# Performance work log

Hardware: AMD Instinct MI355X
Metric: run time of the kernel (lower is better)

The kernel has to match this reference:

```python
import jax, jax.numpy as jnp
import numpy as np

B, N, D = 16, 4096, 128
M = 2048  # codebook size
EPS = 1e-10


def setup_inputs() -> dict:
    key = jax.random.key(0)
    kx, kw = jax.random.split(key)
    x = jax.random.normal(kx, (B, N, D), dtype=jnp.float32)
    # codebook (nn.Embedding weight, kaiming-uniform init ~ uniform(-bound, bound))
    bound = np.sqrt(6.0 / D)
    weight = jax.random.uniform(kw, (M, D), dtype=jnp.float32, minval=-bound, maxval=bound)
    return {"x": x, "weight": weight}


def reference(x, weight):
    b, n, d = x.shape
    m = weight.shape[0]
    q = x.reshape(b * n, d)                       # (bn, d)
    # squared L2 distances: ||q||^2 + ||k||^2 - 2 q.k  (temperature==0 -> argmax of -dist)
    l2_q = jnp.sum(q * q, axis=1, keepdims=True)  # (bn, 1)
    l2_k = jnp.sum(weight * weight, axis=1)       # (m,)
    sim = q @ weight.T                            # (bn, m)  GEMM
    dist = l2_q + l2_k - 2.0 * sim
    indices = jnp.argmin(dist, axis=1)            # (bn,)
    z = weight[indices]                           # onehot @ k == gather
    quantized = z.reshape(b, n, d)
    # straight-through estimator (training path): q + (z - q).detach()
    quantized_st = x + jax.lax.stop_gradient(quantized - x)
    # commitment loss: mse(quantized.detach(), x)
    loss = jnp.mean((jax.lax.stop_gradient(quantized_st) - x) ** 2)
    # perplexity over codebook usage (h == 1 head)
    counts = jnp.zeros((m,), dtype=x.dtype).at[indices].add(1.0)
    p = counts / (b * n)                          # mean of onehot over (b, n)
    perp = jnp.exp(-jnp.sum(p * jnp.log(p + EPS)))[None]  # shape (1,) == 'h'
    out_indices = indices.reshape(b, 1, n)
    return quantized_st, loss, perp, out_indices
```

## Files before the change

### kernel.cpp

```cpp
#include <hip/hip_runtime.h>
#include <hip/hip_bf16.h>
#include <math.h>

#define D_DIM 128
#define M_CODES 2048
#define BN_TOT 65536
#define OUT_LOSS 8388608
#define OUT_PERP 8388609
#define OUT_IDX 8388610
#define MARGIN 2e-3f

#define QB 64

#define WS_L2K 0
#define WS_PB 8192
#define WS_IDX 1056768
#define WS_PART 1318912
#define WS_CNT 1351680
#define WS_FLAGCNT 1359872
#define WS_FLAGGED 1360896

typedef __bf16 bf16x8 __attribute__((ext_vector_type(8)));
typedef float f32x4 __attribute__((ext_vector_type(4)));

#define GLOAD_LDS16(g, l)                                         \
  __builtin_amdgcn_global_load_lds(                               \
      (const __attribute__((address_space(1))) void*)(g),         \
      (__attribute__((address_space(3))) void*)(l), 16, 0, 0)

#define MFMA16(a, b, c) __builtin_amdgcn_mfma_f32_16x16x32_bf16((a), (b), (c), 0, 0, 0)

__global__ __launch_bounds__(256) void prep_kernel(const float* __restrict__ w,
                                                   float* __restrict__ l2k,
                                                   __bf16* __restrict__ pb,
                                                   int* __restrict__ counts,
                                                   int* __restrict__ flagcnt) {
  int gid = blockIdx.x * 256 + threadIdx.x;

  if (gid < M_CODES) {
    const float4* p = (const float4*)(w + (size_t)gid * D_DIM);
    double s = 0.0;
#pragma unroll
    for (int j = 0; j < 32; ++j) {
      float4 v = p[j];
      s += (double)(v.x * v.x);
      s += (double)(v.y * v.y);
      s += (double)(v.z * v.z);
      s += (double)(v.w * v.w);
    }
    l2k[gid] = (float)s;
    counts[gid] = 0;
    if (gid == 0) *flagcnt = 0;
  }

  int lane = gid & 63;
  int g = gid >> 6;
  int cid = g & 15;
  int p = g >> 4;
  int k2 = cid & 7;
  int ks = k2 >> 1;
  int wc = k2 & 1;
  int code = p * 32 + wc * 16 + (lane & 15);
  int koff = ks * 32 + (lane >> 4) * 8;
  const float* src = w + (size_t)code * D_DIM + koff;
  float4 u = *(const float4*)src;
  float4 v = *(const float4*)(src + 4);
  float f[8] = {u.x, u.y, u.z, u.w, v.x, v.y, v.z, v.w};
  bf16x8 o;
#pragma unroll
  for (int j = 0; j < 8; ++j) {
    __bf16 hh = (__bf16)f[j];
    o[j] = (cid < 8) ? hh : (__bf16)(f[j] - (float)hh);
  }
  *(bf16x8*)(pb + (size_t)g * 512 + lane * 8) = o;
}

__device__ __forceinline__ void merge_bs(float& b, float& s, int& i,
                                         float ob, float os, int oi) {
  if (ob > b) {
    s = fmaxf(b, os);
    b = ob;
    i = oi;
  } else if (ob < b) {
    s = fmaxf(s, ob);
  } else {
    s = b;
    if (oi < i) i = oi;
  }
}

__global__ __launch_bounds__(256, 2) void argmin_mfma(
    const float* __restrict__ x, const __bf16* __restrict__ pb,
    const float* __restrict__ l2k, int* __restrict__ best_idx,
    int* __restrict__ flag_count, int* __restrict__ flagged) {
  __shared__ __align__(16) unsigned char ldsB[2 * 32768];
  __shared__ float redB[4][32];
  __shared__ float redS[4][32];
  __shared__ int redI[4][32];

  const int tid = threadIdx.x;
  const int wv = tid >> 6;
  const int lane = tid & 63;
  const int col = lane & 15;
  const int quad = lane >> 4;
  const int wc = wv & 1;
  const int wq = wv >> 1;
  const int q0 = blockIdx.x * QB;

  bf16x8 ah[2][4], al[2][4];
#pragma unroll
  for (int mt = 0; mt < 2; ++mt) {
#pragma unroll
    for (int ks = 0; ks < 4; ++ks) {
      const float* xr =
          x + (size_t)(q0 + wq * 32 + 16 * mt + col) * D_DIM + 32 * ks + 8 * quad;
      float4 u = *(const float4*)xr;
      float4 v = *(const float4*)(xr + 4);
      float f[8] = {u.x, u.y, u.z, u.w, v.x, v.y, v.z, v.w};
      bf16x8 h, l;
#pragma unroll
      for (int j = 0; j < 8; ++j) {
        __bf16 hh = (__bf16)f[j];
        h[j] = hh;
        l[j] = (__bf16)(f[j] - (float)hh);
      }
      ah[mt][ks] = h;
      al[mt][ks] = l;
    }
  }

  float m1[2][4], m2[2][4];
  int bp[2][4];
#pragma unroll
  for (int mt = 0; mt < 2; ++mt)
#pragma unroll
    for (int r = 0; r < 4; ++r) {
      m1[mt][r] = -3.4e38f;
      m2[mt][r] = -3.4e38f;
      bp[mt][r] = 0;
    }

  const int ldsw = wc * 1024 + lane * 16;
  const float* l2p = l2k + wc * 16 + col;

  auto stage = [&](int ch, unsigned char* db) {
    const char* s = (const char*)pb + (size_t)ch * 32768 + wv * 8192 + lane * 16;
#pragma unroll
    for (int i = 0; i < 8; ++i) GLOAD_LDS16(s + i * 1024, db + i * 1024);
  };

  stage(0, ldsB + wv * 8192);
  float l2a = l2p[0];
  float l2b = l2p[32];
  __syncthreads();

#pragma unroll 1
  for (int ch = 0; ch < 32; ++ch) {
    const int buf = ch & 1;
    if (ch < 31) stage(ch + 1, ldsB + (buf ^ 1) * 32768 + wv * 8192);
    float l2na = 0.f, l2nb = 0.f;
    if (ch < 31) {
      l2na = l2p[(2 * ch + 2) * 32];
      l2nb = l2p[(2 * ch + 3) * 32];
    }

    const unsigned char* rb = ldsB + buf * 32768 + ldsw;
    float ia = -0.5f * l2a, ib = -0.5f * l2b;
    f32x4 a00 = (f32x4){ia, ia, ia, ia};
    f32x4 a10 = (f32x4){ia, ia, ia, ia};
    f32x4 a01 = (f32x4){ib, ib, ib, ib};
    f32x4 a11 = (f32x4){ib, ib, ib, ib};

    bf16x8 h0 = *(const bf16x8*)(rb);
    bf16x8 l0 = *(const bf16x8*)(rb + 8192);
    bf16x8 h1 = *(const bf16x8*)(rb + 16384);
    bf16x8 l1 = *(const bf16x8*)(rb + 24576);

#define DO_KS(KS, PRE)                                                    \
    {                                                                     \
      bf16x8 nh0, nl0, nh1, nl1;                                          \
      if (PRE) {                                                          \
        nh0 = *(const bf16x8*)(rb + ((KS) + 1) * 2048);                   \
        nl0 = *(const bf16x8*)(rb + 8192 + ((KS) + 1) * 2048);            \
        nh1 = *(const bf16x8*)(rb + 16384 + ((KS) + 1) * 2048);           \
        nl1 = *(const bf16x8*)(rb + 24576 + ((KS) + 1) * 2048);           \
      }                                                                   \
      a00 = MFMA16(al[0][KS], h0, a00);                                   \
      a10 = MFMA16(al[1][KS], h0, a10);                                   \
      a01 = MFMA16(al[0][KS], h1, a01);                                   \
      a11 = MFMA16(al[1][KS], h1, a11);                                   \
      a00 = MFMA16(ah[0][KS], l0, a00);                                   \
      a10 = MFMA16(ah[1][KS], l0, a10);                                   \
      a01 = MFMA16(ah[0][KS], l1, a01);                                   \
      a11 = MFMA16(ah[1][KS], l1, a11);                                   \
      a00 = MFMA16(ah[0][KS], h0, a00);                                   \
      a10 = MFMA16(ah[1][KS], h0, a10);                                   \
      a01 = MFMA16(ah[0][KS], h1, a01);                                   \
      a11 = MFMA16(ah[1][KS], h1, a11);                                   \
      if (PRE) { h0 = nh0; l0 = nl0; h1 = nh1; l1 = nl1; }                \
    }
    DO_KS(0, 1)
    DO_KS(1, 1)
    DO_KS(2, 1)
    DO_KS(3, 0)
#undef DO_KS

#pragma unroll
    for (int mt = 0; mt < 2; ++mt) {
#pragma unroll
      for (int r = 0; r < 4; ++r) {
        float dd = (mt == 0) ? a00[r] : a10[r];
        bool gt = dd > m1[mt][r];
        m2[mt][r] = fmaxf(m2[mt][r], fminf(m1[mt][r], dd));
        bp[mt][r] = gt ? (ch * 2 + 0) : bp[mt][r];
        m1[mt][r] = fmaxf(m1[mt][r], dd);
      }
    }
#pragma unroll
    for (int mt = 0; mt < 2; ++mt) {
#pragma unroll
      for (int r = 0; r < 4; ++r) {
        float dd = (mt == 0) ? a01[r] : a11[r];
        bool gt = dd > m1[mt][r];
        m2[mt][r] = fmaxf(m2[mt][r], fminf(m1[mt][r], dd));
        bp[mt][r] = gt ? (ch * 2 + 1) : bp[mt][r];
        m1[mt][r] = fmaxf(m1[mt][r], dd);
      }
    }

    l2a = l2na;
    l2b = l2nb;
    __syncthreads();
  }

#pragma unroll
  for (int mt = 0; mt < 2; ++mt) {
#pragma unroll
    for (int r = 0; r < 4; ++r) {
      float b = m1[mt][r], s = m2[mt][r];
      int i = bp[mt][r] * 32 + wc * 16 + col;
#pragma unroll
      for (int m = 1; m < 16; m <<= 1) {
        float ob = __shfl_xor(b, m);
        float os = __shfl_xor(s, m);
        int oi = __shfl_xor(i, m);
        merge_bs(b, s, i, ob, os, oi);
      }
      if (col == 0) {
        int qloc = 16 * mt + 4 * quad + r;
        redB[wv][qloc] = b;
        redS[wv][qloc] = s;
        redI[wv][qloc] = i;
      }
    }
  }
  __syncthreads();

  if (tid < QB) {
    int wq2 = tid >> 5;
    int ql = tid & 31;
    float b = -3.4e38f, s = -3.4e38f;
    int i = 0x7fffffff;
    merge_bs(b, s, i, redB[wq2 * 2 + 0][ql], redS[wq2 * 2 + 0][ql], redI[wq2 * 2 + 0][ql]);
    merge_bs(b, s, i, redB[wq2 * 2 + 1][ql], redS[wq2 * 2 + 1][ql], redI[wq2 * 2 + 1][ql]);
    best_idx[q0 + tid] = i;
    if (2.0f * (b - s) < MARGIN) {
      int pos = atomicAdd(flag_count, 1);
      flagged[pos] = q0 + tid;
    }
  }
}

__global__ __launch_bounds__(256) void fixup_kernel(const float* __restrict__ x,
                                                    const float* __restrict__ w,
                                                    const float* __restrict__ l2k32,
                                                    const int* __restrict__ flagged,
                                                    const int* __restrict__ flag_count,
                                                    int* __restrict__ best_idx) {
  __shared__ float qs[D_DIM];
  __shared__ float l2q_sh;
  __shared__ float redD[256];
  __shared__ int redI[256];
  const int tid = threadIdx.x;
  const int n = *flag_count;
  for (int f = blockIdx.x; f < n; f += gridDim.x) {
    __syncthreads();
    int q = flagged[f];
    if (tid < D_DIM) qs[tid] = x[(size_t)q * D_DIM + tid];
    __syncthreads();
    if (tid == 0) {
      double s = 0.0;
      for (int d = 0; d < D_DIM; ++d) {
        float t = qs[d] * qs[d];
        s += (double)t;
      }
      l2q_sh = (float)s;
    }
    __syncthreads();
    const float l2q = l2q_sh;
    float bd = 3.4e38f;
    int bi = 0x7fffffff;
    for (int c = tid; c < M_CODES; c += 256) {
      const float4* wr = (const float4*)(w + (size_t)c * D_DIM);
      double s = 0.0;
#pragma unroll
      for (int j = 0; j < 32; ++j) {
        float4 v = wr[j];
        s = fma((double)qs[j * 4 + 0], (double)v.x, s);
        s = fma((double)qs[j * 4 + 1], (double)v.y, s);
        s = fma((double)qs[j * 4 + 2], (double)v.z, s);
        s = fma((double)qs[j * 4 + 3], (double)v.w, s);
      }
      float simf = (float)s;
      float S = l2q + l2k32[c];
      float T = 2.0f * simf;
      float dist = S - T;
      if (dist < bd) { bd = dist; bi = c; }
    }
    redD[tid] = bd;
    redI[tid] = bi;
    __syncthreads();
    for (int off = 128; off; off >>= 1) {
      if (tid < off) {
        float od = redD[tid + off];
        int oi = redI[tid + off];
        if (od < redD[tid] || (od == redD[tid] && oi < redI[tid])) {
          redD[tid] = od;
          redI[tid] = oi;
        }
      }
      __syncthreads();
    }
    if (tid == 0) best_idx[q] = redI[0];
  }
}

__global__ __launch_bounds__(256) void epilogue_kernel(const float* __restrict__ x,
                                                       const float* __restrict__ w,
                                                       const int* __restrict__ best_idx,
                                                       float* __restrict__ out,
                                                       float* __restrict__ part,
                                                       int* __restrict__ counts) {
  int gid = blockIdx.x * 256 + threadIdx.x;
  int q = gid >> 5;
  int d4 = gid & 31;
  int idx = best_idx[q];
  float4 xv = ((const float4*)x)[gid];
  float4 wv = ((const float4*)w)[(size_t)idx * 32 + d4];
  float4 o;
  float t0 = wv.x - xv.x; o.x = xv.x + t0; float e0 = o.x - xv.x;
  float t1 = wv.y - xv.y; o.y = xv.y + t1; float e1 = o.y - xv.y;
  float t2 = wv.z - xv.z; o.z = xv.z + t2; float e2 = o.z - xv.z;
  float t3 = wv.w - xv.w; o.w = xv.w + t3; float e3 = o.w - xv.w;
  float ls = e0 * e0 + e1 * e1 + e2 * e2 + e3 * e3;
  ((float4*)out)[gid] = o;

  for (int off = 32; off; off >>= 1) ls += __shfl_down(ls, off);
  __shared__ float red[4];
  if ((threadIdx.x & 63) == 0) red[threadIdx.x >> 6] = ls;
  __syncthreads();
  if (threadIdx.x == 0) part[blockIdx.x] = red[0] + red[1] + red[2] + red[3];

  if (d4 == 0) {
    out[OUT_IDX + q] = (float)idx;
    atomicAdd(&counts[idx], 1);
  }
}

__global__ __launch_bounds__(256) void finalize_kernel(const int* __restrict__ counts,
                                                       const float* __restrict__ part,
                                                       float* __restrict__ out) {
  int tid = threadIdx.x;
  float ls = 0.f;
  for (int i = tid; i < 8192; i += 256) ls += part[i];
  float es = 0.f;
  for (int i = tid; i < M_CODES; i += 256) {
    float p = (float)counts[i] * (1.0f / 65536.0f);
    es += p * logf(p + 1e-10f);
  }
  for (int off = 32; off; off >>= 1) {
    ls += __shfl_down(ls, off);
    es += __shfl_down(es, off);
  }
  __shared__ float redl[4], rede[4];
  if ((tid & 63) == 0) {
    redl[tid >> 6] = ls;
    rede[tid >> 6] = es;
  }
  __syncthreads();
  if (tid == 0) {
    out[OUT_LOSS] = (redl[0] + redl[1] + redl[2] + redl[3]) * (1.0f / 8388608.0f);
    out[OUT_PERP] = expf(-(rede[0] + rede[1] + rede[2] + rede[3]));
  }
}

extern "C" void kernel_launch(void* const* d_in, const int* in_sizes, int n_in,
                              void* d_out, int out_size, void* d_ws, size_t ws_size,
                              hipStream_t stream) {
  const float* x = (const float*)d_in[0];
  const float* w = (const float*)d_in[1];
  float* out = (float*)d_out;
  char* ws = (char*)d_ws;
  float* l2k = (float*)(ws + WS_L2K);
  __bf16* pb = (__bf16*)(ws + WS_PB);
  int* bidx = (int*)(ws + WS_IDX);
  float* part = (float*)(ws + WS_PART);
  int* counts = (int*)(ws + WS_CNT);
  int* flagcnt = (int*)(ws + WS_FLAGCNT);
  int* flagged = (int*)(ws + WS_FLAGGED);

  prep_kernel<<<256, 256, 0, stream>>>(w, l2k, pb, counts, flagcnt);
  argmin_mfma<<<BN_TOT / QB, 256, 0, stream>>>(x, pb, l2k, bidx, flagcnt, flagged);
  fixup_kernel<<<256, 256, 0, stream>>>(x, w, l2k, flagged, flagcnt, bidx);
  epilogue_kernel<<<8192, 256, 0, stream>>>(x, w, bidx, out, part, counts);
  finalize_kernel<<<1, 256, 0, stream>>>(counts, part, out);
}
```

Measured before the change: 248.1 us.

## Software-pipeline argmin fold with MFMA and interleave staged loads per k-step

Restructures the main MFMA loop so that the argmin fold of the previous chunk's accumulators runs interleaved with the current chunk's MFMAs, using ping-pong accumulator sets. Global-to-LDS staging of the next chunk is split across the four k-steps with explicit waitcnt, raw s_barrier and sched_barrier plus setprio around MFMA bursts. The codebook norms are pre-scaled by -0.5 into LDS once per block instead of being read from global memory each chunk. It adds more barriers per chunk and higher register pressure from the doubled accumulators.

```diff
diff --git a/kernel.cpp b/kernel.cpp
--- a/kernel.cpp
+++ b/kernel.cpp
@@ -89,11 +89,97 @@
   }
 }
 
+__device__ __forceinline__ void fold4(const f32x4& f, float (&m1r)[4],
+                                      float (&m2r)[4], int (&bpr)[4], int pid) {
+#pragma unroll
+  for (int r = 0; r < 4; ++r) {
+    float dd = f[r];
+    bool gt = dd > m1r[r];
+    m2r[r] = fmaxf(m2r[r], fminf(m1r[r], dd));
+    bpr[r] = gt ? pid : bpr[r];
+    m1r[r] = fmaxf(m1r[r], dd);
+  }
+}
+
+#define MFMA_KS(KS, H0, L0, H1, L1)                                   \
+  A00 = MFMA16(al[0][KS], H0, A00); A10 = MFMA16(al[1][KS], H0, A10); \
+  A01 = MFMA16(al[0][KS], H1, A01); A11 = MFMA16(al[1][KS], H1, A11); \
+  A00 = MFMA16(ah[0][KS], L0, A00); A10 = MFMA16(ah[1][KS], L0, A10); \
+  A01 = MFMA16(ah[0][KS], L1, A01); A11 = MFMA16(ah[1][KS], L1, A11); \
+  A00 = MFMA16(ah[0][KS], H0, A00); A10 = MFMA16(ah[1][KS], H0, A10); \
+  A01 = MFMA16(ah[0][KS], H1, A01); A11 = MFMA16(ah[1][KS], H1, A11);
+
+template <int DOFOLD, int DOSTAGE>
+__device__ __forceinline__ void chunk_body(
+    int CH, int PREV, unsigned char* ldsBp, const char* pbase, int ldsw, int wv,
+    const bf16x8 (&ah)[2][4], const bf16x8 (&al)[2][4],
+    f32x4& A00, f32x4& A10, f32x4& A01, f32x4& A11,
+    const f32x4& F00, const f32x4& F10, const f32x4& F01, const f32x4& F11,
+    float ia, float ib,
+    float (&m1)[2][4], float (&m2)[2][4], int (&bp)[2][4]) {
+  const unsigned char* rb = ldsBp + (CH & 1) * 32768 + ldsw;
+  unsigned char* db = ldsBp + ((CH & 1) ^ 1) * 32768 + wv * 8192;
+  const char* sg = pbase + (size_t)(CH + 1) * 32768;
+
+  if (DOSTAGE) {
+    GLOAD_LDS16(sg, db);
+    GLOAD_LDS16(sg + 1024, db + 1024);
+    asm volatile("s_waitcnt vmcnt(2)" ::: "memory");
+  } else {
+    asm volatile("s_waitcnt vmcnt(0)" ::: "memory");
+  }
+  __builtin_amdgcn_s_barrier();
+  {
+    bf16x8 h0 = *(const bf16x8*)(rb);
+    bf16x8 l0 = *(const bf16x8*)(rb + 8192);
+    bf16x8 h1 = *(const bf16x8*)(rb + 16384);
+    bf16x8 l1 = *(const bf16x8*)(rb + 24576);
+    asm volatile("s_waitcnt lgkmcnt(0)" ::: "memory");
+    __builtin_amdgcn_sched_barrier(0);
+    A00 = (f32x4){ia, ia, ia, ia};
+    A10 = (f32x4){ia, ia, ia, ia};
+    A01 = (f32x4){ib, ib, ib, ib};
+    A11 = (f32x4){ib, ib, ib, ib};
+    __builtin_amdgcn_s_setprio(1);
+    MFMA_KS(0, h0, l0, h1, l1)
+    __builtin_amdgcn_s_setprio(0);
+  }
+  if (DOFOLD) fold4(F00, m1[0], m2[0], bp[0], PREV * 2 + 0);
+  __builtin_amdgcn_s_barrier();
+
+#pragma unroll
+  for (int k = 1; k < 4; ++k) {
+    bf16x8 h0 = *(const bf16x8*)(rb + k * 2048);
+    bf16x8 l0 = *(const bf16x8*)(rb + 8192 + k * 2048);
+    bf16x8 h1 = *(const bf16x8*)(rb + 16384 + k * 2048);
+    bf16x8 l1 = *(const bf16x8*)(rb + 24576 + k * 2048);
+    if (DOSTAGE) {
+      GLOAD_LDS16(sg + (2 * k) * 1024, db + (2 * k) * 1024);
+      GLOAD_LDS16(sg + (2 * k + 1) * 1024, db + (2 * k + 1) * 1024);
+    }
+    __builtin_amdgcn_s_barrier();
+    asm volatile("s_waitcnt lgkmcnt(0)" ::: "memory");
+    __builtin_amdgcn_sched_barrier(0);
+    __builtin_amdgcn_s_setprio(1);
+    if (k == 1) { MFMA_KS(1, h0, l0, h1, l1) }
+    else if (k == 2) { MFMA_KS(2, h0, l0, h1, l1) }
+    else { MFMA_KS(3, h0, l0, h1, l1) }
+    __builtin_amdgcn_s_setprio(0);
+    if (DOFOLD) {
+      if (k == 1) fold4(F10, m1[1], m2[1], bp[1], PREV * 2 + 0);
+      else if (k == 2) fold4(F01, m1[0], m2[0], bp[0], PREV * 2 + 1);
+      else fold4(F11, m1[1], m2[1], bp[1], PREV * 2 + 1);
+    }
+    __builtin_amdgcn_s_barrier();
+  }
+}
+
 __global__ __launch_bounds__(256, 2) void argmin_mfma(
     const float* __restrict__ x, const __bf16* __restrict__ pb,
     const float* __restrict__ l2k, int* __restrict__ best_idx,
     int* __restrict__ flag_count, int* __restrict__ flagged) {
   __shared__ __align__(16) unsigned char ldsB[2 * 32768];
+  __shared__ float l2s[2048];
   __shared__ float redB[4][32];
   __shared__ float redS[4][32];
   __shared__ int redI[4][32];
@@ -129,6 +215,15 @@
     }
   }
 
+  {
+    float4 a = ((const float4*)l2k)[2 * tid];
+    float4 b = ((const float4*)l2k)[2 * tid + 1];
+    float4 na = {-0.5f * a.x, -0.5f * a.y, -0.5f * a.z, -0.5f * a.w};
+    float4 nb = {-0.5f * b.x, -0.5f * b.y, -0.5f * b.z, -0.5f * b.w};
+    ((float4*)l2s)[2 * tid] = na;
+    ((float4*)l2s)[2 * tid + 1] = nb;
+  }
+
   float m1[2][4], m2[2][4];
   int bp[2][4];
 #pragma unroll
@@ -141,97 +236,56 @@
     }
 
   const int ldsw = wc * 1024 + lane * 16;
-  const float* l2p = l2k + wc * 16 + col;
-
-  auto stage = [&](int ch, unsigned char* db) {
-    const char* s = (const char*)pb + (size_t)ch * 32768 + wv * 8192 + lane * 16;
-#pragma unroll
-    for (int i = 0; i < 8; ++i) GLOAD_LDS16(s + i * 1024, db + i * 1024);
-  };
-
-  stage(0, ldsB + wv * 8192);
-  float l2a = l2p[0];
-  float l2b = l2p[32];
+  const int wcol = wc * 16 + col;
+  const char* pbase = (const char*)pb + wv * 8192 + lane * 16;
+
+  {
+    unsigned char* d0 = ldsB + wv * 8192;
+#pragma unroll
+    for (int i = 0; i < 8; ++i) GLOAD_LDS16(pbase + i * 1024, d0 + i * 1024);
+  }
   __syncthreads();
 
+  f32x4 pA00 = {0, 0, 0, 0}, pA10 = {0, 0, 0, 0}, pA01 = {0, 0, 0, 0}, pA11 = {0, 0, 0, 0};
+  f32x4 pB00 = {0, 0, 0, 0}, pB10 = {0, 0, 0, 0}, pB01 = {0, 0, 0, 0}, pB11 = {0, 0, 0, 0};
+
+  float ia = l2s[wcol];
+  float ib = l2s[wcol + 32];
+
+  chunk_body<0, 1>(0, 0, ldsB, pbase, ldsw, wv, ah, al,
+                   pA00, pA10, pA01, pA11, pB00, pB10, pB01, pB11,
+                   ia, ib, m1, m2, bp);
+  ia = l2s[64 + wcol];
+  ib = l2s[96 + wcol];
+
 #pragma unroll 1
-  for (int ch = 0; ch < 32; ++ch) {
-    const int buf = ch & 1;
-    if (ch < 31) stage(ch + 1, ldsB + (buf ^ 1) * 32768 + wv * 8192);
-    float l2na = 0.f, l2nb = 0.f;
-    if (ch < 31) {
-      l2na = l2p[(2 * ch + 2) * 32];
-      l2nb = l2p[(2 * ch + 3) * 32];
-    }
-
-    const unsigned char* rb = ldsB + buf * 32768 + ldsw;
-    float ia = -0.5f * l2a, ib = -0.5f * l2b;
-    f32x4 a00 = (f32x4){ia, ia, ia, ia};
-    f32x4 a10 = (f32x4){ia, ia, ia, ia};
-    f32x4 a01 = (f32x4){ib, ib, ib, ib};
-    f32x4 a11 = (f32x4){ib, ib, ib, ib};
-
-    bf16x8 h0 = *(const bf16x8*)(rb);
-    bf16x8 l0 = *(const bf16x8*)(rb + 8192);
-    bf16x8 h1 = *(const bf16x8*)(rb + 16384);
-    bf16x8 l1 = *(const bf16x8*)(rb + 24576);
-
-#define DO_KS(KS, PRE)                                                    \
-    {                                                                     \
-      bf16x8 nh0, nl0, nh1, nl1;                                          \
-      if (PRE) {                                                          \
-        nh0 = *(const bf16x8*)(rb + ((KS) + 1) * 2048);                   \
-        nl0 = *(const bf16x8*)(rb + 8192 + ((KS) + 1) * 2048);            \
-        nh1 = *(const bf16x8*)(rb + 16384 + ((KS) + 1) * 2048);           \
-        nl1 = *(const bf16x8*)(rb + 24576 + ((KS) + 1) * 2048);           \
-      }                                                                   \
-      a00 = MFMA16(al[0][KS], h0, a00);                                   \
-      a10 = MFMA16(al[1][KS], h0, a10);                                   \
-      a01 = MFMA16(al[0][KS], h1, a01);                                   \
-      a11 = MFMA16(al[1][KS], h1, a11);                                   \
-      a00 = MFMA16(ah[0][KS], l0, a00);                                   \
-      a10 = MFMA16(ah[1][KS], l0, a10);                                   \
-      a01 = MFMA16(ah[0][KS], l1, a01);                                   \
-      a11 = MFMA16(ah[1][KS], l1, a11);                                   \
-      a00 = MFMA16(ah[0][KS], h0, a00);                                   \
-      a10 = MFMA16(ah[1][KS], h0, a10);                                   \
-      a01 = MFMA16(ah[0][KS], h1, a01);                                   \
-      a11 = MFMA16(ah[1][KS], h1, a11);                                   \
-      if (PRE) { h0 = nh0; l0 = nl0; h1 = nh1; l1 = nl1; }                \
-    }
-    DO_KS(0, 1)
-    DO_KS(1, 1)
-    DO_KS(2, 1)
-    DO_KS(3, 0)
-#undef DO_KS
-
-#pragma unroll
-    for (int mt = 0; mt < 2; ++mt) {
-#pragma unroll
-      for (int r = 0; r < 4; ++r) {
-        float dd = (mt == 0) ? a00[r] : a10[r];
-        bool gt = dd > m1[mt][r];
-        m2[mt][r] = fmaxf(m2[mt][r], fminf(m1[mt][r], dd));
-        bp[mt][r] = gt ? (ch * 2 + 0) : bp[mt][r];
-        m1[mt][r] = fmaxf(m1[mt][r], dd);
-      }
-    }
-#pragma unroll
-    for (int mt = 0; mt < 2; ++mt) {
-#pragma unroll
-      for (int r = 0; r < 4; ++r) {
-        float dd = (mt == 0) ? a01[r] : a11[r];
-        bool gt = dd > m1[mt][r];
-        m2[mt][r] = fmaxf(m2[mt][r], fminf(m1[mt][r], dd));
-        bp[mt][r] = gt ? (ch * 2 + 1) : bp[mt][r];
-        m1[mt][r] = fmaxf(m1[mt][r], dd);
-      }
-    }
-
-    l2a = l2na;
-    l2b = l2nb;
-    __syncthreads();
-  }
+  for (int ch = 1; ch <= 29; ch += 2) {
+    chunk_body<1, 1>(ch, ch - 1, ldsB, pbase, ldsw, wv, ah, al,
+                     pB00, pB10, pB01, pB11, pA00, pA10, pA01, pA11,
+                     ia, ib, m1, m2, bp);
+    {
+      int b0 = (ch + 1) * 64 + wcol;
+      ia = l2s[b0];
+      ib = l2s[b0 + 32];
+    }
+    chunk_body<1, 1>(ch + 1, ch, ldsB, pbase, ldsw, wv, ah, al,
+                     pA00, pA10, pA01, pA11, pB00, pB10, pB01, pB11,
+                     ia, ib, m1, m2, bp);
+    {
+      int b0 = (ch + 2) * 64 + wcol;
+      ia = l2s[b0];
+      ib = l2s[b0 + 32];
+    }
+  }
+
+  chunk_body<1, 0>(31, 30, ldsB, pbase, ldsw, wv, ah, al,
+                   pB00, pB10, pB01, pB11, pA00, pA10, pA01, pA11,
+                   ia, ib, m1, m2, bp);
+
+  fold4(pB00, m1[0], m2[0], bp[0], 62);
+  fold4(pB10, m1[1], m2[1], bp[1], 62);
+  fold4(pB01, m1[0], m2[0], bp[0], 63);
+  fold4(pB11, m1[1], m2[1], bp[1], 63);
 
 #pragma unroll
   for (int mt = 0; mt < 2; ++mt) {
```

Result: slower. 260.8 us (+5.1%).
